# Kernel tuning notes

Measured on AMD Instinct MI355X. Metric: run time of the kernel, lower is better.

## Reference

```python
import jax, jax.numpy as jnp
import numpy as np


def setup_inputs() -> dict:
    key = jax.random.key(0)
    k1, k2, k3 = jax.random.split(key, 3)
    Na, Nb, D, K = 1024, 1024, 512, 256
    a = jax.random.normal(k1, (Na, D), dtype=jnp.float32)
    b = jax.random.normal(k2, (Nb, D), dtype=jnp.float32)
    feats = jax.random.normal(k3, (K, D), dtype=jnp.float32)
    return {"a": a, "b": b, "feats": feats}


def reference(a, b, feats):
    # 'ignorematch' mode of the Difference module.
    # Project both sets onto the feature bank: [Na,K] and [Nb,K]
    a_fk = jnp.matmul(a, feats.T)          # [Na, K]
    b_fk = jnp.matmul(b, feats.T)          # [Nb, K]
    a_e = a_fk[:, None, :]                 # [Na, 1, K]
    b_e = b_fk[None, :, :]                 # [1, Nb, K]
    # features present in a (>0) but absent in b (<=0)
    mask = ((a_e > 0) & (b_e <= 0)).astype(a_fk.dtype)  # [Na, Nb, K]
    result = jnp.sum(a_e * mask, axis=2)   # [Na, Nb]
    return result
```

## Files before the change

### kernel.cpp

```cpp
#include <hip/hip_runtime.h>
#include <hip/hip_fp16.h>


typedef _Float16 f16;
typedef _Float16 f16x8 __attribute__((ext_vector_type(8)));
typedef _Float16 f16x4 __attribute__((ext_vector_type(4)));
typedef float    f32x4 __attribute__((ext_vector_type(4)));

__global__ __launch_bounds__(256) void convert_kernel(
    const float* __restrict__ a, const float* __restrict__ b,
    const float* __restrict__ feats,
    f16* __restrict__ Xh, f16* __restrict__ Xl,
    f16* __restrict__ Fh, f16* __restrict__ Fl)
{
    const int g   = blockIdx.x * 256 + threadIdx.x;
    const int row = g >> 7;
    const int c4  = (g & 127) * 4;

    const float* src;
    f16 *oh, *ol;
    if (row < 1024) {
        src = a + (size_t)row * 512 + c4;
        oh = Xh + (size_t)row * 512 + c4;  ol = Xl + (size_t)row * 512 + c4;
    } else if (row < 2048) {
        src = b + (size_t)(row - 1024) * 512 + c4;
        oh = Xh + (size_t)row * 512 + c4;  ol = Xl + (size_t)row * 512 + c4;
    } else {
        const int r = row - 2048;
        src = feats + (size_t)r * 512 + c4;
        oh = Fh + (size_t)r * 512 + c4;    ol = Fl + (size_t)r * 512 + c4;
    }

    float4 v = *(const float4*)src;
    float vv[4] = {v.x, v.y, v.z, v.w};
    f16x4 h, l;
    #pragma unroll
    for (int i = 0; i < 4; i++) {
        f16 hi = (f16)vv[i];
        float r = vv[i] - (float)hi;
        h[i] = hi;
        l[i] = (f16)(r * 2048.0f);
    }
    *(f16x4*)oh = h;
    *(f16x4*)ol = l;
}

__global__ __launch_bounds__(512) void stage1_kernel(
    const f16* __restrict__ Xh, const f16* __restrict__ Xl,
    const f16* __restrict__ Fh, const f16* __restrict__ Fl,
    f16* __restrict__ P, f16* __restrict__ M)
{
    const int mt = blockIdx.x >> 2;
    const int nt = blockIdx.x & 3;
    const int m0 = mt * 32;
    const int n0 = nt * 64;

    const int tid  = threadIdx.x;
    const int w    = tid >> 6;
    const int lane = tid & 63;
    const int wr   = w >> 2;
    const int wc   = w & 3;
    const int l15  = lane & 15;
    const int q    = lane >> 4;

    const int arow = m0 + wr * 16 + l15;
    const int brow = n0 + wc * 16 + l15;

    const f16* pa_h = Xh + (size_t)arow * 512 + q * 8;
    const f16* pa_l = Xl + (size_t)arow * 512 + q * 8;
    const f16* pf_h = Fh + (size_t)brow * 512 + q * 8;
    const f16* pf_l = Fl + (size_t)brow * 512 + q * 8;

    f32x4 acc1  = {0.f, 0.f, 0.f, 0.f};

    if (m0 >= 1024) {
        f32x4 acc2a = {0.f, 0.f, 0.f, 0.f};
        f32x4 acc2b = {0.f, 0.f, 0.f, 0.f};
        #pragma unroll
        for (int c = 0; c < 16; c++) {
            f16x8 ah = *(const f16x8*)(pa_h + c * 32);
            f16x8 al = *(const f16x8*)(pa_l + c * 32);
            f16x8 fh = *(const f16x8*)(pf_h + c * 32);
            f16x8 fl = *(const f16x8*)(pf_l + c * 32);
            acc1  = __builtin_amdgcn_mfma_f32_16x16x32_f16(ah, fh, acc1,  0, 0, 0);
            acc2a = __builtin_amdgcn_mfma_f32_16x16x32_f16(ah, fl, acc2a, 0, 0, 0);
            acc2b = __builtin_amdgcn_mfma_f32_16x16x32_f16(al, fh, acc2b, 0, 0, 0);
        }
        const int orow0 = (m0 - 1024) + wr * 16 + q * 4;
        const int ocol  = n0 + wc * 16 + l15;
        #pragma unroll
        for (int r = 0; r < 4; r++) {
            float v = acc1[r] + (acc2a[r] + acc2b[r]) * (1.0f / 2048.0f);
            M[(size_t)(orow0 + r) * 256 + ocol] = (f16)((v <= 0.0f) ? 1.0f : 0.0f);
        }
    } else {
        #pragma unroll
        for (int c = 0; c < 16; c++) {
            f16x8 ah = *(const f16x8*)(pa_h + c * 32);
            f16x8 fh = *(const f16x8*)(pf_h + c * 32);
            acc1 = __builtin_amdgcn_mfma_f32_16x16x32_f16(ah, fh, acc1, 0, 0, 0);
        }
        const int orow0 = m0 + wr * 16 + q * 4;
        const int ocol  = n0 + wc * 16 + l15;
        #pragma unroll
        for (int r = 0; r < 4; r++) {
            float v = fmaxf(acc1[r], 0.0f);
            P[(size_t)(orow0 + r) * 256 + ocol] = (f16)v;
        }
    }
}

__global__ __launch_bounds__(256) void gemm2_kernel(
    const f16* __restrict__ p, const f16* __restrict__ m,
    float* __restrict__ out)
{
    const int bi = blockIdx.x >> 4;
    const int bj = blockIdx.x & 15;
    const int i0 = bi * 32;
    const int j0 = bj * 64;

    const int tid  = threadIdx.x;
    const int w    = tid >> 6;
    const int lane = tid & 63;
    const int wi = w >> 1;
    const int wj = w & 1;

    const int l15 = lane & 15;
    const int q   = lane >> 4;

    const int arow  = i0 + wi * 16 + l15;
    const int jbase = j0 + wj * 32;
    const int brow0 = jbase + l15;
    const int brow1 = brow0 + 16;

    f32x4 acc0 = {0.f, 0.f, 0.f, 0.f};
    f32x4 acc1 = {0.f, 0.f, 0.f, 0.f};

    #pragma unroll
    for (int k0 = 0; k0 < 256; k0 += 32) {
        const int ko = k0 + q * 8;
        f16x8 av = *(const f16x8*)(p + (size_t)arow  * 256 + ko);
        f16x8 b0 = *(const f16x8*)(m + (size_t)brow0 * 256 + ko);
        f16x8 b1 = *(const f16x8*)(m + (size_t)brow1 * 256 + ko);
        acc0 = __builtin_amdgcn_mfma_f32_16x16x32_f16(av, b0, acc0, 0, 0, 0);
        acc1 = __builtin_amdgcn_mfma_f32_16x16x32_f16(av, b1, acc1, 0, 0, 0);
    }

    const int orow = i0 + wi * 16 + q * 4;
    const int ocol = jbase + l15;
    #pragma unroll
    for (int r = 0; r < 4; r++) {
        out[(size_t)(orow + r) * 1024 + ocol]      = acc0[r];
        out[(size_t)(orow + r) * 1024 + ocol + 16] = acc1[r];
    }
}

extern "C" void kernel_launch(void* const* d_in, const int* in_sizes, int n_in,
                              void* d_out, int out_size, void* d_ws, size_t ws_size,
                              hipStream_t stream) {
    const float* a     = (const float*)d_in[0];
    const float* b     = (const float*)d_in[1];
    const float* feats = (const float*)d_in[2];
    float* out = (float*)d_out;

    f16* Xh = (f16*)d_ws;
    f16* Xl = Xh + (size_t)2048 * 512;
    f16* Fh = Xl + (size_t)2048 * 512;
    f16* Fl = Fh + (size_t)256 * 512;
    f16* P  = Fl + (size_t)256 * 512;
    f16* M  = P  + (size_t)1024 * 256;

    convert_kernel<<<1152, 256, 0, stream>>>(a, b, feats, Xh, Xl, Fh, Fl);
    stage1_kernel <<< 256, 512, 0, stream>>>(Xh, Xl, Fh, Fl, P, M);
    gemm2_kernel  <<< 512, 256, 0, stream>>>(P, M, out);
}
```

Before: 84.25 us.

## Fuse conversion, projection and masked GEMM into one cooperative kernel

Replaces the three launches (fp32→fp16 split conversion, projection GEMM, masked GEMM) with one cooperative kernel. The split into high and low fp16 parts now happens in registers on the fly, so the intermediate Xh/Xl/Fh/Fl buffers are never written. The P/M intermediates are stored in the tail of the output buffer. Two grid syncs separate the phases: one after writing P/M, and one after every block has loaded its operands into registers, so the output can safely overwrite the scratch region. This removes launch gaps and conversion traffic, but each block reloads fp32 rows redundantly and pays for two grid-wide barriers.

```diff
diff --git a/kernel.cpp b/kernel.cpp
--- a/kernel.cpp
+++ b/kernel.cpp
@@ -1,153 +1,137 @@
 #include <hip/hip_runtime.h>
 #include <hip/hip_fp16.h>
+#include <hip/hip_cooperative_groups.h>
+
+namespace cg = cooperative_groups;
 
 
 typedef _Float16 f16;
 typedef _Float16 f16x8 __attribute__((ext_vector_type(8)));
-typedef _Float16 f16x4 __attribute__((ext_vector_type(4)));
 typedef float    f32x4 __attribute__((ext_vector_type(4)));
 
-__global__ __launch_bounds__(256) void convert_kernel(
+__global__ __launch_bounds__(512) void fused_kernel(
     const float* __restrict__ a, const float* __restrict__ b,
-    const float* __restrict__ feats,
-    f16* __restrict__ Xh, f16* __restrict__ Xl,
-    f16* __restrict__ Fh, f16* __restrict__ Fl)
+    const float* __restrict__ feats, float* out)
 {
-    const int g   = blockIdx.x * 256 + threadIdx.x;
-    const int row = g >> 7;
-    const int c4  = (g & 127) * 4;
+    f16* P = (f16*)(out + (size_t)768 * 1024);
+    f16* M = P + (size_t)1024 * 256;
 
-    const float* src;
-    f16 *oh, *ol;
-    if (row < 1024) {
-        src = a + (size_t)row * 512 + c4;
-        oh = Xh + (size_t)row * 512 + c4;  ol = Xl + (size_t)row * 512 + c4;
-    } else if (row < 2048) {
-        src = b + (size_t)(row - 1024) * 512 + c4;
-        oh = Xh + (size_t)row * 512 + c4;  ol = Xl + (size_t)row * 512 + c4;
-    } else {
-        const int r = row - 2048;
-        src = feats + (size_t)r * 512 + c4;
-        oh = Fh + (size_t)r * 512 + c4;    ol = Fl + (size_t)r * 512 + c4;
-    }
-
-    float4 v = *(const float4*)src;
-    float vv[4] = {v.x, v.y, v.z, v.w};
-    f16x4 h, l;
-    #pragma unroll
-    for (int i = 0; i < 4; i++) {
-        f16 hi = (f16)vv[i];
-        float r = vv[i] - (float)hi;
-        h[i] = hi;
-        l[i] = (f16)(r * 2048.0f);
-    }
-    *(f16x4*)oh = h;
-    *(f16x4*)ol = l;
-}
-
-__global__ __launch_bounds__(512) void stage1_kernel(
-    const f16* __restrict__ Xh, const f16* __restrict__ Xl,
-    const f16* __restrict__ Fh, const f16* __restrict__ Fl,
-    f16* __restrict__ P, f16* __restrict__ M)
-{
-    const int mt = blockIdx.x >> 2;
-    const int nt = blockIdx.x & 3;
-    const int m0 = mt * 32;
-    const int n0 = nt * 64;
-
+    const int bid  = blockIdx.x;
     const int tid  = threadIdx.x;
     const int w    = tid >> 6;
     const int lane = tid & 63;
-    const int wr   = w >> 2;
-    const int wc   = w & 3;
     const int l15  = lane & 15;
     const int q    = lane >> 4;
 
-    const int arow = m0 + wr * 16 + l15;
-    const int brow = n0 + wc * 16 + l15;
+    {
+        const int mt = bid >> 2;
+        const int nt = bid & 3;
+        const int m0 = mt * 32;
+        const int n0 = nt * 64;
+        const int wr = w >> 2;
+        const int wc = w & 3;
 
-    const f16* pa_h = Xh + (size_t)arow * 512 + q * 8;
-    const f16* pa_l = Xl + (size_t)arow * 512 + q * 8;
-    const f16* pf_h = Fh + (size_t)brow * 512 + q * 8;
-    const f16* pf_l = Fl + (size_t)brow * 512 + q * 8;
+        const int arow = m0 + wr * 16 + l15;
+        const int brow = n0 + wc * 16 + l15;
+        const float* xrow = (arow < 1024) ? (a + (size_t)arow * 512)
+                                          : (b + (size_t)(arow - 1024) * 512);
+        const float* frow = feats + (size_t)brow * 512;
 
-    f32x4 acc1  = {0.f, 0.f, 0.f, 0.f};
-
-    if (m0 >= 1024) {
-        f32x4 acc2a = {0.f, 0.f, 0.f, 0.f};
-        f32x4 acc2b = {0.f, 0.f, 0.f, 0.f};
-        #pragma unroll
-        for (int c = 0; c < 16; c++) {
-            f16x8 ah = *(const f16x8*)(pa_h + c * 32);
-            f16x8 al = *(const f16x8*)(pa_l + c * 32);
-            f16x8 fh = *(const f16x8*)(pf_h + c * 32);
-            f16x8 fl = *(const f16x8*)(pf_l + c * 32);
-            acc1  = __builtin_amdgcn_mfma_f32_16x16x32_f16(ah, fh, acc1,  0, 0, 0);
-            acc2a = __builtin_amdgcn_mfma_f32_16x16x32_f16(ah, fl, acc2a, 0, 0, 0);
-            acc2b = __builtin_amdgcn_mfma_f32_16x16x32_f16(al, fh, acc2b, 0, 0, 0);
-        }
-        const int orow0 = (m0 - 1024) + wr * 16 + q * 4;
-        const int ocol  = n0 + wc * 16 + l15;
-        #pragma unroll
-        for (int r = 0; r < 4; r++) {
-            float v = acc1[r] + (acc2a[r] + acc2b[r]) * (1.0f / 2048.0f);
-            M[(size_t)(orow0 + r) * 256 + ocol] = (f16)((v <= 0.0f) ? 1.0f : 0.0f);
-        }
-    } else {
-        #pragma unroll
-        for (int c = 0; c < 16; c++) {
-            f16x8 ah = *(const f16x8*)(pa_h + c * 32);
-            f16x8 fh = *(const f16x8*)(pf_h + c * 32);
-            acc1 = __builtin_amdgcn_mfma_f32_16x16x32_f16(ah, fh, acc1, 0, 0, 0);
-        }
-        const int orow0 = m0 + wr * 16 + q * 4;
-        const int ocol  = n0 + wc * 16 + l15;
-        #pragma unroll
-        for (int r = 0; r < 4; r++) {
-            float v = fmaxf(acc1[r], 0.0f);
-            P[(size_t)(orow0 + r) * 256 + ocol] = (f16)v;
+        f32x4 s1 = {0.f, 0.f, 0.f, 0.f};
+        if (m0 >= 1024) {
+            f32x4 s2 = {0.f, 0.f, 0.f, 0.f};
+            f32x4 s3 = {0.f, 0.f, 0.f, 0.f};
+            #pragma unroll
+            for (int c = 0; c < 16; c++) {
+                const int off = c * 32 + q * 8;
+                float4 x0 = *(const float4*)(xrow + off);
+                float4 x1 = *(const float4*)(xrow + off + 4);
+                float4 f0 = *(const float4*)(frow + off);
+                float4 f1 = *(const float4*)(frow + off + 4);
+                float xs[8] = {x0.x, x0.y, x0.z, x0.w, x1.x, x1.y, x1.z, x1.w};
+                float fs[8] = {f0.x, f0.y, f0.z, f0.w, f1.x, f1.y, f1.z, f1.w};
+                f16x8 ah, al, fh, fl;
+                #pragma unroll
+                for (int j = 0; j < 8; j++) {
+                    f16 h = (f16)xs[j];
+                    ah[j] = h;
+                    al[j] = (f16)((xs[j] - (float)h) * 2048.0f);
+                    f16 g = (f16)fs[j];
+                    fh[j] = g;
+                    fl[j] = (f16)((fs[j] - (float)g) * 2048.0f);
+                }
+                s1 = __builtin_amdgcn_mfma_f32_16x16x32_f16(ah, fh, s1, 0, 0, 0);
+                s2 = __builtin_amdgcn_mfma_f32_16x16x32_f16(ah, fl, s2, 0, 0, 0);
+                s3 = __builtin_amdgcn_mfma_f32_16x16x32_f16(al, fh, s3, 0, 0, 0);
+            }
+            const int orow0 = (m0 - 1024) + wr * 16 + q * 4;
+            const int ocol  = n0 + wc * 16 + l15;
+            #pragma unroll
+            for (int r = 0; r < 4; r++) {
+                float v = s1[r] + (s2[r] + s3[r]) * (1.0f / 2048.0f);
+                M[(size_t)(orow0 + r) * 256 + ocol] = (f16)((v <= 0.f) ? 1.f : 0.f);
+            }
+        } else {
+            #pragma unroll
+            for (int c = 0; c < 16; c++) {
+                const int off = c * 32 + q * 8;
+                float4 x0 = *(const float4*)(xrow + off);
+                float4 x1 = *(const float4*)(xrow + off + 4);
+                float4 f0 = *(const float4*)(frow + off);
+                float4 f1 = *(const float4*)(frow + off + 4);
+                float xs[8] = {x0.x, x0.y, x0.z, x0.w, x1.x, x1.y, x1.z, x1.w};
+                float fs[8] = {f0.x, f0.y, f0.z, f0.w, f1.x, f1.y, f1.z, f1.w};
+                f16x8 ah, fh;
+                #pragma unroll
+                for (int j = 0; j < 8; j++) {
+                    ah[j] = (f16)xs[j];
+                    fh[j] = (f16)fs[j];
+                }
+                s1 = __builtin_amdgcn_mfma_f32_16x16x32_f16(ah, fh, s1, 0, 0, 0);
+            }
+            const int orow0 = m0 + wr * 16 + q * 4;
+            const int ocol  = n0 + wc * 16 + l15;
+            #pragma unroll
+            for (int r = 0; r < 4; r++) {
+                float v = fmaxf(s1[r], 0.f);
+                P[(size_t)(orow0 + r) * 256 + ocol] = (f16)v;
+            }
         }
     }
-}
 
-__global__ __launch_bounds__(256) void gemm2_kernel(
-    const f16* __restrict__ p, const f16* __restrict__ m,
-    float* __restrict__ out)
-{
-    const int bi = blockIdx.x >> 4;
-    const int bj = blockIdx.x & 15;
-    const int i0 = bi * 32;
+    cg::this_grid().sync();
+
+    const int bi = bid >> 4;
+    const int bj = bid & 15;
+    const int i0 = bi * 64;
     const int j0 = bj * 64;
-
-    const int tid  = threadIdx.x;
-    const int w    = tid >> 6;
-    const int lane = tid & 63;
     const int wi = w >> 1;
     const int wj = w & 1;
+    const int arow2 = i0 + wi * 16 + l15;
+    const int jb    = j0 + wj * 32;
+    const int brow0 = jb + l15;
+    const int brow1 = brow0 + 16;
 
-    const int l15 = lane & 15;
-    const int q   = lane >> 4;
+    f16x8 fa[8], g0[8], g1[8];
+    #pragma unroll
+    for (int kc = 0; kc < 8; kc++) {
+        const int ko = kc * 32 + q * 8;
+        fa[kc] = *(const f16x8*)(P + (size_t)arow2 * 256 + ko);
+        g0[kc] = *(const f16x8*)(M + (size_t)brow0 * 256 + ko);
+        g1[kc] = *(const f16x8*)(M + (size_t)brow1 * 256 + ko);
+    }
 
-    const int arow  = i0 + wi * 16 + l15;
-    const int jbase = j0 + wj * 32;
-    const int brow0 = jbase + l15;
-    const int brow1 = brow0 + 16;
+    cg::this_grid().sync();
 
     f32x4 acc0 = {0.f, 0.f, 0.f, 0.f};
     f32x4 acc1 = {0.f, 0.f, 0.f, 0.f};
-
     #pragma unroll
-    for (int k0 = 0; k0 < 256; k0 += 32) {
-        const int ko = k0 + q * 8;
-        f16x8 av = *(const f16x8*)(p + (size_t)arow  * 256 + ko);
-        f16x8 b0 = *(const f16x8*)(m + (size_t)brow0 * 256 + ko);
-        f16x8 b1 = *(const f16x8*)(m + (size_t)brow1 * 256 + ko);
-        acc0 = __builtin_amdgcn_mfma_f32_16x16x32_f16(av, b0, acc0, 0, 0, 0);
-        acc1 = __builtin_amdgcn_mfma_f32_16x16x32_f16(av, b1, acc1, 0, 0, 0);
+    for (int kc = 0; kc < 8; kc++) {
+        acc0 = __builtin_amdgcn_mfma_f32_16x16x32_f16(fa[kc], g0[kc], acc0, 0, 0, 0);
+        acc1 = __builtin_amdgcn_mfma_f32_16x16x32_f16(fa[kc], g1[kc], acc1, 0, 0, 0);
     }
-
     const int orow = i0 + wi * 16 + q * 4;
-    const int ocol = jbase + l15;
+    const int ocol = jb + l15;
     #pragma unroll
     for (int r = 0; r < 4; r++) {
         out[(size_t)(orow + r) * 1024 + ocol]      = acc0[r];
@@ -162,15 +146,9 @@
     const float* b     = (const float*)d_in[1];
     const float* feats = (const float*)d_in[2];
     float* out = (float*)d_out;
+    (void)d_ws; (void)ws_size;
 
-    f16* Xh = (f16*)d_ws;
-    f16* Xl = Xh + (size_t)2048 * 512;
-    f16* Fh = Xl + (size_t)2048 * 512;
-    f16* Fl = Fh + (size_t)256 * 512;
-    f16* P  = Fl + (size_t)256 * 512;
-    f16* M  = P  + (size_t)1024 * 256;
-
-    convert_kernel<<<1152, 256, 0, stream>>>(a, b, feats, Xh, Xl, Fh, Fl);
-    stage1_kernel <<< 256, 512, 0, stream>>>(Xh, Xl, Fh, Fl, P, M);
-    gemm2_kernel  <<< 512, 256, 0, stream>>>(P, M, out);
+    void* args[4] = {(void*)&a, (void*)&b, (void*)&feats, (void*)&out};
+    hipLaunchCooperativeKernel((void*)fused_kernel, dim3(256), dim3(512),
+                               args, 0, stream);
 }
```

Result: slower. 135.8 us (+61.1%).
